# Performance work log

Measured on AMD Instinct MI355X. Metric: run time of the kernel, lower is better.

Reference implementation:

```python
import jax, jax.numpy as jnp
import numpy as np

MAX_CACHE_LEN = 4096


def _rotate_half(t):
    d = t.shape[-1] // 2
    return jnp.concatenate([-t[..., d:], t[..., :d]], axis=-1)


def _apply_rope(t, cos, sin):
    # t: (B, S, H, D); cos/sin: (S, D)
    c = cos[None, :, None, :]
    s = sin[None, :, None, :]
    return t * c + _rotate_half(t) * s


def setup_inputs() -> dict:
    key = jax.random.key(0)
    ks = jax.random.split(key, 7)
    B, S, E, D, KVH = 1, 2048, 2048, 64, 8
    sc = 0.02
    x = jax.random.normal(ks[0], (B, S, E), dtype=jnp.float32)
    Wq = jax.random.normal(ks[1], (E, E), dtype=jnp.float32) * sc
    Wk = jax.random.normal(ks[2], (KVH * D, E), dtype=jnp.float32) * sc
    Wv = jax.random.normal(ks[3], (KVH * D, E), dtype=jnp.float32) * sc
    Wo = jax.random.normal(ks[4], (E, E), dtype=jnp.float32) * sc
    # RoPE tables
    pos = jnp.arange(S, dtype=jnp.float32)[:, None]
    inv_freq = 1.0 / (10000.0 ** (jnp.arange(0, D, 2, dtype=jnp.float32) / D))
    ang = pos * inv_freq[None, :]              # (S, D/2)
    ang = jnp.concatenate([ang, ang], axis=-1)  # (S, D)
    cos = jnp.cos(ang)
    sin = jnp.sin(ang)
    # additive causal mask (1,1,S,S): 0 where allowed, -1e9 where masked
    causal = jnp.tril(jnp.ones((S, S), dtype=bool))
    attn_mask = jnp.where(causal, 0.0, -1e9).astype(jnp.float32)[None, None]
    return {"x": x, "Wq": Wq, "Wk": Wk, "Wv": Wv, "Wo": Wo,
            "cos": cos, "sin": sin, "attn_mask": attn_mask, "last_pos": S}


def reference(x, Wq, Wk, Wv, Wo, cos, sin, attn_mask, last_pos):
    B, S, E = x.shape
    D = cos.shape[-1]
    H = E // D
    KVH = Wk.shape[0] // D
    group = H // KVH

    q = (x @ Wq.T).reshape(B, S, H, D)
    k = (x @ Wk.T).reshape(B, S, KVH, D)
    v = (x @ Wv.T).reshape(B, S, KVH, D)

    q = _apply_rope(q, cos, sin)
    k = _apply_rope(k, cos, sin)

    # KV-cache write (index_copy at positions [last_pos-S, last_pos)), then slice [:last_pos]
    key_cache = jnp.zeros((B, MAX_CACHE_LEN, KVH, D), dtype=x.dtype)
    value_cache = jnp.zeros((B, MAX_CACHE_LEN, KVH, D), dtype=x.dtype)
    key_cache = jax.lax.dynamic_update_slice(key_cache, jax.lax.stop_gradient(k), (0, last_pos - S, 0, 0))
    value_cache = jax.lax.dynamic_update_slice(value_cache, jax.lax.stop_gradient(v), (0, last_pos - S, 0, 0))
    kc = key_cache[:, :last_pos]    # (B, T, KVH, D)
    vc = value_cache[:, :last_pos]

    # GQA: repeat kv heads to match q heads
    kc = jnp.repeat(kc, group, axis=2)  # (B, T, H, D)
    vc = jnp.repeat(vc, group, axis=2)

    scale = 1.0 / np.sqrt(D)
    scores = jnp.einsum('bqhd,bkhd->bhqk', q, kc) * scale
    scores = scores + attn_mask
    probs = jax.nn.softmax(scores.astype(jnp.float32), axis=-1).astype(x.dtype)
    attn = jnp.einsum('bhqk,bkhd->bqhd', probs, vc)  # (B, S, H, D)
    out = attn.reshape(B, S, E) @ Wo.T
    return out
```

## Files before the change

### kernel.cpp

```cpp
#include <hip/hip_runtime.h>
#include <stdint.h>

typedef unsigned short u16;
typedef unsigned int   u32;

typedef __bf16 bf16x8 __attribute__((ext_vector_type(8)));
typedef float  fx4    __attribute__((ext_vector_type(4)));
typedef u16    u16x8  __attribute__((ext_vector_type(8)));
typedef u16    u16x4  __attribute__((ext_vector_type(4)));

typedef __attribute__((address_space(1))) unsigned int as1_u32;
typedef __attribute__((address_space(3))) unsigned int as3_u32;

__device__ __forceinline__ void gload_lds16(const void* g, void* lds) {
  __builtin_amdgcn_global_load_lds((const as1_u32*)(uintptr_t)g,
                                   (as3_u32*)(uintptr_t)lds, 16, 0, 0);
}

__device__ __forceinline__ float b2f(u32 bits) {
  union { u32 i; float f; } v; v.i = bits << 16; return v.f;
}
__device__ __forceinline__ u16 f2b(float f) {
  union { float f; u32 i; } v; v.f = f;
  u32 x = v.i;
  return (u16)((x + 0x7fffu + ((x >> 16) & 1u)) >> 16);
}
__device__ __forceinline__ u16 f2b_hw(float f) {
  union { __bf16 b; u16 u; } v; v.b = (__bf16)f; return v.u;
}
__device__ __forceinline__ float exp2_hw(float f) {
  return __builtin_amdgcn_exp2f(f);
}
__device__ __forceinline__ u32 cvtpk_bf16(float a, float b) {
  u32 r;
  asm("v_cvt_pk_bf16_f32 %0, %1, %2" : "=v"(r) : "v"(a), "v"(b));
  return r;
}

__global__ __launch_bounds__(256) void cast_kernel(
    const float* __restrict__ s0, const float* __restrict__ s1,
    const float* __restrict__ s2, const float* __restrict__ s3,
    const float* __restrict__ s4, u16* __restrict__ dst)
{
  const size_t i8 = ((size_t)blockIdx.x * 256 + threadIdx.x) * 8;
  if (i8 >= 14680064) return;
  const float* src; size_t off;
  if      (i8 <  4194304) { src = s0; off = i8; }
  else if (i8 <  8388608) { src = s1; off = i8 - 4194304; }
  else if (i8 <  9437184) { src = s2; off = i8 - 8388608; }
  else if (i8 < 10485760) { src = s3; off = i8 - 9437184; }
  else                    { src = s4; off = i8 - 10485760; }
  const float4 a = *(const float4*)(src + off);
  const float4 b = *(const float4*)(src + off + 4);
  u16x8 o;
  o[0] = f2b(a.x); o[1] = f2b(a.y); o[2] = f2b(a.z); o[3] = f2b(a.w);
  o[4] = f2b(b.x); o[5] = f2b(b.y); o[6] = f2b(b.z); o[7] = f2b(b.w);
  *(u16x8*)(dst + i8) = o;
}

template <int MODE>
__global__ __launch_bounds__(512) void gemm_bt(
    const u16* __restrict__ A, const u16* __restrict__ B0,
    const u16* __restrict__ B1, const u16* __restrict__ B2,
    void* __restrict__ Cv, int K, int split1, int split2, int ldc,
    const float* __restrict__ cosb, const float* __restrict__ sinb,
    u16* __restrict__ vtg)
{
  __shared__ __align__(16) u16 smem[5 * 8192];

  const int n0 = blockIdx.x * 128;
  const int m0 = blockIdx.y * 128;

  const u16* Bsel; int nb;
  if (n0 < split1)      { Bsel = B0; nb = n0; }
  else if (n0 < split2) { Bsel = B1; nb = n0 - split1; }
  else                  { Bsel = B2; nb = n0 - split2; }

  const int tid  = threadIdx.x;
  const int wave = tid >> 6, lane = tid & 63;
  const int wm = wave >> 1, wn = wave & 1;
  const int quad = lane >> 4, l16 = lane & 15;

  fx4 acc[2][4];
#pragma unroll
  for (int i = 0; i < 2; ++i)
#pragma unroll
    for (int j = 0; j < 4; ++j) acc[i][j] = fx4{0.f, 0.f, 0.f, 0.f};

  const int row = tid >> 2;
  const int ch  = tid & 3;
  const int csw = (ch ^ ((row >> 1) & 3)) * 8;
  auto stage = [&](int kt, int buf) {
    u16* As = smem + buf * 8192;
    u16* Bs = As + 4096;
    const int k0 = kt * 32;
    gload_lds16(A    + (size_t)(m0 + row) * K + k0 + csw, As + tid * 8);
    gload_lds16(Bsel + (size_t)(nb + row) * K + k0 + csw, Bs + tid * 8);
  };

  const int KT = K >> 5;
  stage(0, 0); stage(1, 1); stage(2, 2); stage(3, 3);
  int bufR = 0, bufW = 4;

  const int fx = (l16 >> 1) & 3;
  const int cA = (quad ^ fx) * 8;

#pragma unroll 1
  for (int kt = 0; kt < KT; ++kt) {
    const int rem = KT - 1 - kt;
    if (rem >= 3)      asm volatile("s_waitcnt vmcnt(6)\n\ts_barrier" ::: "memory");
    else if (rem == 2) asm volatile("s_waitcnt vmcnt(4)\n\ts_barrier" ::: "memory");
    else if (rem == 1) asm volatile("s_waitcnt vmcnt(2)\n\ts_barrier" ::: "memory");
    else               asm volatile("s_waitcnt vmcnt(0)\n\ts_barrier" ::: "memory");
    if (kt + 4 < KT) stage(kt + 4, bufW);

    const u16* As = smem + bufR * 8192;
    const u16* Bs = As + 4096;

    bf16x8 af[2], bfr[4];
#pragma unroll
    for (int t = 0; t < 2; ++t)
      af[t]  = *(const bf16x8*)&As[(wm * 32 + t * 16 + l16) * 32 + cA];
#pragma unroll
    for (int t = 0; t < 4; ++t)
      bfr[t] = *(const bf16x8*)&Bs[(wn * 64 + t * 16 + l16) * 32 + cA];
#pragma unroll
    for (int ti = 0; ti < 2; ++ti)
#pragma unroll
      for (int tj = 0; tj < 4; ++tj)
        acc[ti][tj] = __builtin_amdgcn_mfma_f32_16x16x32_bf16(
            af[ti], bfr[tj], acc[ti][tj], 0, 0, 0);

    bufR = (bufR == 4) ? 0 : bufR + 1;
    bufW = (bufW == 4) ? 0 : bufW + 1;
  }

  if (MODE == 1) {
    float* C = (float*)Cv;
#pragma unroll
    for (int ti = 0; ti < 2; ++ti) {
      const int row_b = m0 + wm * 32 + ti * 16 + quad * 4;
#pragma unroll
      for (int tj = 0; tj < 4; ++tj) {
        const int col = n0 + wn * 64 + tj * 16 + l16;
#pragma unroll
        for (int r = 0; r < 4; ++r)
          C[(size_t)(row_b + r) * ldc + col] = acc[ti][tj][r];
      }
    }
  } else {
    u16* C = (u16*)Cv;
    const int cb = n0 + wn * 64;
    if (cb < 2560) {
      const float qs = (cb < 2048) ? 0.18033688f : 1.0f;
#pragma unroll
      for (int ti = 0; ti < 2; ++ti) {
#pragma unroll
        for (int r = 0; r < 4; ++r) {
          const int s = m0 + wm * 32 + ti * 16 + quad * 4 + r;
          const float* cr = cosb + s * 64;
          const float* sr = sinb + s * 64;
          u16* orow = C + (size_t)s * 3072 + cb;
#pragma unroll
          for (int tj = 0; tj < 2; ++tj) {
            const int d0 = tj * 16 + l16, d1 = d0 + 32;
            const float x0 = acc[ti][tj][r], x1 = acc[ti][tj + 2][r];
            orow[d0] = f2b((x0 * cr[d0] - x1 * sr[d0]) * qs);
            orow[d1] = f2b((x1 * cr[d1] + x0 * sr[d1]) * qs);
          }
        }
      }
    } else {
      const int vr0 = cb - 2560;
#pragma unroll
      for (int ti = 0; ti < 2; ++ti) {
        const int s0 = m0 + wm * 32 + ti * 16 + quad * 4;
#pragma unroll
        for (int tj = 0; tj < 4; ++tj) {
          const int vr = vr0 + tj * 16 + l16;
          u16x4 o;
#pragma unroll
          for (int r = 0; r < 4; ++r) o[r] = f2b(acc[ti][tj][r]);
          *(u16x4*)(vtg + (size_t)vr * 2048 + s0) = o;
        }
      }
    }
  }
}

__global__ __launch_bounds__(256) void attn_kernel(
    const u16* __restrict__ qkv, const u16* __restrict__ vt,
    u16* __restrict__ attnbuf)
{
  const int bi  = blockIdx.x;
  const int kvh = bi & 7;
  const int j   = bi >> 3;
  const int h   = kvh * 4 + (j & 3);
  const int bx  = 31 - (j >> 2);
  const int tid = threadIdx.x;
  const int w = tid >> 6, lane = tid & 63;
  const int quad = lane >> 4, l16 = lane & 15;

  __shared__ __align__(16) u16 Qs[64 * 64];
  __shared__ __align__(16) u16 Kb[2][64 * 64];
  __shared__ __align__(16) u16 Vb[2][64 * 64];
  __shared__ __align__(16) u32 Ps[4][16 * 32];

  const int r0    = bx * 64;
  const int nhalf = bx + 1;
  const int kcol  = 2048 + kvh * 64;

  const int srow = tid >> 3;
  const int sc   = tid & 7;

  auto stageQ = [&]() {
#pragma unroll
    for (int i = 0; i < 2; ++i) {
      const int r  = srow + i * 32;
      const int cs = sc ^ (r & 7);
      gload_lds16(qkv + (size_t)(r0 + r) * 3072 + h * 64 + cs * 8,
                  Qs + (size_t)(tid + i * 256) * 8);
    }
  };
  auto stageKV = [&](int n) {
    const int k0 = n * 64;
    u16* Kd = Kb[n & 1];
    u16* Vd = Vb[n & 1];
#pragma unroll
    for (int i = 0; i < 2; ++i) {
      const int r  = srow + i * 32;
      const int cs = sc ^ (r & 7);
      gload_lds16(qkv + (size_t)(k0 + r) * 3072 + kcol + cs * 8,
                  Kd + (size_t)(tid + i * 256) * 8);
      gload_lds16(vt + (size_t)(kvh * 64 + r) * 2048 + k0 + cs * 8,
                  Vd + (size_t)(tid + i * 256) * 8);
    }
  };

  stageQ();
  stageKV(0);
  asm volatile("s_waitcnt vmcnt(0)\n\ts_barrier" ::: "memory");

  const int xm = l16 & 7;
  const int qrow = w * 16 + l16;
  const bf16x8 aq0 = *(const bf16x8*)&Qs[qrow * 64 + ((quad    ) ^ xm) * 8];
  const bf16x8 aq1 = *(const bf16x8*)&Qs[qrow * 64 + ((4 + quad) ^ xm) * 8];

  fx4 O[4];
  float l_acc = 0.f;
#pragma unroll
  for (int c = 0; c < 4; ++c) O[c] = fx4{0.f, 0.f, 0.f, 0.f};

  const int s2 = (l16 & 7) << 1;

#pragma unroll 1
  for (int n = 0; n < nhalf; ++n) {
    if (n + 1 < nhalf) stageKV(n + 1);
    const u16* Kh = Kb[n & 1];
    const u16* Vd = Vb[n & 1];
    const int k0h = n * 64;

    fx4 sc4[4];
    __builtin_amdgcn_s_setprio(1);
#pragma unroll
    for (int c = 0; c < 4; ++c) {
      const int kr = c * 16 + l16;
      const bf16x8 b0 = *(const bf16x8*)&Kh[kr * 64 + ((quad    ) ^ xm) * 8];
      const bf16x8 b1 = *(const bf16x8*)&Kh[kr * 64 + ((4 + quad) ^ xm) * 8];
      fx4 z = fx4{0.f, 0.f, 0.f, 0.f};
      z      = __builtin_amdgcn_mfma_f32_16x16x32_bf16(b0, aq0, z, 0, 0, 0);
      sc4[c] = __builtin_amdgcn_mfma_f32_16x16x32_bf16(b1, aq1, z, 0, 0, 0);
    }
    __builtin_amdgcn_s_setprio(0);

    const int qg16 = r0 + w * 16 + l16;
    if (k0h >= r0) {
#pragma unroll
      for (int c = 0; c < 4; ++c)
#pragma unroll
        for (int r = 0; r < 4; ++r) {
          float p = exp2_hw(sc4[c][r]);
          if (k0h + c * 16 + quad * 4 + r > qg16) p = 0.f;
          l_acc += p;
          sc4[c][r] = p;
        }
    } else {
#pragma unroll
      for (int c = 0; c < 4; ++c)
#pragma unroll
        for (int r = 0; r < 4; ++r) {
          const float p = exp2_hw(sc4[c][r]);
          l_acc += p;
          sc4[c][r] = p;
        }
    }

#pragma unroll
    for (int c = 0; c < 4; ++c) {
      const u32 lo = cvtpk_bf16(sc4[c][0], sc4[c][1]);
      const u32 hi = cvtpk_bf16(sc4[c][2], sc4[c][3]);
      const int c2 = (c * 4 + quad) ^ s2;
      *(uint2*)&Ps[w][l16 * 32 + 2 * c2] = uint2{lo, hi};
    }

    const bf16x8 ap0 = *(const bf16x8*)&Ps[w][l16 * 32 + 2 * ((2 * quad    ) ^ s2)];
    const bf16x8 ap1 = *(const bf16x8*)&Ps[w][l16 * 32 + 2 * ((8 + 2 * quad) ^ s2)];
    __builtin_amdgcn_s_setprio(1);
#pragma unroll
    for (int c = 0; c < 4; ++c) {
      const int vr = c * 16 + l16;
      const bf16x8 v0 = *(const bf16x8*)&Vd[vr * 64 + ((quad    ) ^ xm) * 8];
      const bf16x8 v1 = *(const bf16x8*)&Vd[vr * 64 + ((4 + quad) ^ xm) * 8];
      O[c] = __builtin_amdgcn_mfma_f32_16x16x32_bf16(ap0, v0, O[c], 0, 0, 0);
      O[c] = __builtin_amdgcn_mfma_f32_16x16x32_bf16(ap1, v1, O[c], 0, 0, 0);
    }
    __builtin_amdgcn_s_setprio(0);

    asm volatile("s_waitcnt vmcnt(0)\n\ts_barrier" ::: "memory");
  }

  float l = l_acc;
  l += __shfl_xor(l, 16, 64);
  l += __shfl_xor(l, 32, 64);
  const float inv = 1.f / fmaxf(l, 1e-30f);
#pragma unroll
  for (int r = 0; r < 4; ++r) {
    const float iv = __shfl(inv, (lane & 48) | (quad * 4 + r), 64);
    const int qg = r0 + w * 16 + quad * 4 + r;
#pragma unroll
    for (int c = 0; c < 4; ++c)
      attnbuf[(size_t)qg * 2048 + h * 64 + c * 16 + l16] = f2b(O[c][r] * iv);
  }
}

extern "C" void kernel_launch(void* const* d_in, const int* in_sizes, int n_in,
                              void* d_out, int out_size, void* d_ws, size_t ws_size,
                              hipStream_t stream) {
  const float* x    = (const float*)d_in[0];
  const float* Wq   = (const float*)d_in[1];
  const float* Wk   = (const float*)d_in[2];
  const float* Wv   = (const float*)d_in[3];
  const float* Wo   = (const float*)d_in[4];
  const float* cosb = (const float*)d_in[5];
  const float* sinb = (const float*)d_in[6];
  float* out = (float*)d_out;

  u16* ws      = (u16*)d_ws;
  u16* qkv     = ws;
  u16* attnbuf = ws + 6291456;
  u16* xb      = ws + 10485760;
  u16* Wqb     = ws + 14680064;
  u16* Wkb     = ws + 18874368;
  u16* Wvb     = ws + 19922944;
  u16* Wob     = ws + 20971520;
  u16* vtg     = ws + 25165824;

  cast_kernel<<<7168, 256, 0, stream>>>(x, Wq, Wk, Wv, Wo, xb);

  gemm_bt<0><<<dim3(24, 16), 512, 0, stream>>>(
      xb, Wqb, Wkb, Wvb, qkv, 2048, 2048, 2560, 3072, cosb, sinb, vtg);

  attn_kernel<<<1024, 256, 0, stream>>>(qkv, vtg, attnbuf);

  gemm_bt<1><<<dim3(16, 16), 512, 0, stream>>>(
      attnbuf, Wob, Wob, Wob, out, 2048, 1 << 30, 1 << 30, 2048, cosb, sinb, vtg);
}
```

Baseline: 209.9 us.

## Enlarge attention query tile to 128 rows per block for K/V reuse

Each attention block now handles 128 query rows instead of 64, with every wave computing two 16-row groups, so each staged K/V tile feeds twice as many MFMAs and the grid halves to 512 blocks. Q is staged through the K buffer into registers, which frees the separate Q shared-memory array. The block-to-tile mapping is changed to pair long and short causal tiles across the two halves of the grid. This cuts global K/V traffic and barrier count per unit of work, at the cost of more registers per thread and fewer blocks to balance the causal workload.

```diff
diff --git a/kernel.cpp b/kernel.cpp
--- a/kernel.cpp
+++ b/kernel.cpp
@@ -194,34 +194,50 @@
 {
   const int bi  = blockIdx.x;
   const int kvh = bi & 7;
-  const int j   = bi >> 3;
-  const int h   = kvh * 4 + (j & 3);
-  const int bx  = 31 - (j >> 2);
+  const int hs  = (bi >> 3) & 3;
+  const int h   = kvh * 4 + hs;
+  const int g5  = bi >> 5;
+  const int qt  = (bi < 256) ? (15 - g5) : (g5 - 8);
   const int tid = threadIdx.x;
   const int w = tid >> 6, lane = tid & 63;
   const int quad = lane >> 4, l16 = lane & 15;
 
-  __shared__ __align__(16) u16 Qs[64 * 64];
   __shared__ __align__(16) u16 Kb[2][64 * 64];
   __shared__ __align__(16) u16 Vb[2][64 * 64];
-  __shared__ __align__(16) u32 Ps[4][16 * 32];
-
-  const int r0    = bx * 64;
-  const int nhalf = bx + 1;
+  __shared__ __align__(16) u32 Ps[4][2][16 * 32];
+
+  const int r0    = qt * 128;
+  const int nhalf = 2 * qt + 2;
   const int kcol  = 2048 + kvh * 64;
 
   const int srow = tid >> 3;
   const int sc   = tid & 7;
 
-  auto stageQ = [&]() {
-#pragma unroll
-    for (int i = 0; i < 2; ++i) {
+  {
+    u16* Qb = (u16*)Kb;
+#pragma unroll
+    for (int i = 0; i < 4; ++i) {
       const int r  = srow + i * 32;
       const int cs = sc ^ (r & 7);
       gload_lds16(qkv + (size_t)(r0 + r) * 3072 + h * 64 + cs * 8,
-                  Qs + (size_t)(tid + i * 256) * 8);
-    }
-  };
+                  Qb + (size_t)(tid + i * 256) * 8);
+    }
+  }
+  asm volatile("s_waitcnt vmcnt(0)\n\ts_barrier" ::: "memory");
+
+  const int xm = l16 & 7;
+  bf16x8 aq[2][2];
+  {
+    const u16* Qb = (const u16*)Kb;
+#pragma unroll
+    for (int g = 0; g < 2; ++g) {
+      const int qrow = w * 32 + g * 16 + l16;
+      aq[g][0] = *(const bf16x8*)&Qb[qrow * 64 + ((quad    ) ^ xm) * 8];
+      aq[g][1] = *(const bf16x8*)&Qb[qrow * 64 + ((4 + quad) ^ xm) * 8];
+    }
+  }
+  asm volatile("s_waitcnt lgkmcnt(0)\n\ts_barrier" ::: "memory");
+
   auto stageKV = [&](int n) {
     const int k0 = n * 64;
     u16* Kd = Kb[n & 1];
@@ -237,19 +253,15 @@
     }
   };
 
-  stageQ();
   stageKV(0);
   asm volatile("s_waitcnt vmcnt(0)\n\ts_barrier" ::: "memory");
 
-  const int xm = l16 & 7;
-  const int qrow = w * 16 + l16;
-  const bf16x8 aq0 = *(const bf16x8*)&Qs[qrow * 64 + ((quad    ) ^ xm) * 8];
-  const bf16x8 aq1 = *(const bf16x8*)&Qs[qrow * 64 + ((4 + quad) ^ xm) * 8];
-
-  fx4 O[4];
-  float l_acc = 0.f;
-#pragma unroll
-  for (int c = 0; c < 4; ++c) O[c] = fx4{0.f, 0.f, 0.f, 0.f};
+  fx4 O[2][4];
+  float l_acc[2] = {0.f, 0.f};
+#pragma unroll
+  for (int g = 0; g < 2; ++g)
+#pragma unroll
+    for (int c = 0; c < 4; ++c) O[g][c] = fx4{0.f, 0.f, 0.f, 0.f};
 
   const int s2 = (l16 & 7) << 1;
 
@@ -260,76 +272,89 @@
     const u16* Vd = Vb[n & 1];
     const int k0h = n * 64;
 
-    fx4 sc4[4];
+    fx4 sc4[2][4];
     __builtin_amdgcn_s_setprio(1);
 #pragma unroll
     for (int c = 0; c < 4; ++c) {
       const int kr = c * 16 + l16;
       const bf16x8 b0 = *(const bf16x8*)&Kh[kr * 64 + ((quad    ) ^ xm) * 8];
       const bf16x8 b1 = *(const bf16x8*)&Kh[kr * 64 + ((4 + quad) ^ xm) * 8];
-      fx4 z = fx4{0.f, 0.f, 0.f, 0.f};
-      z      = __builtin_amdgcn_mfma_f32_16x16x32_bf16(b0, aq0, z, 0, 0, 0);
-      sc4[c] = __builtin_amdgcn_mfma_f32_16x16x32_bf16(b1, aq1, z, 0, 0, 0);
+#pragma unroll
+      for (int g = 0; g < 2; ++g) {
+        fx4 z = fx4{0.f, 0.f, 0.f, 0.f};
+        z         = __builtin_amdgcn_mfma_f32_16x16x32_bf16(b0, aq[g][0], z, 0, 0, 0);
+        sc4[g][c] = __builtin_amdgcn_mfma_f32_16x16x32_bf16(b1, aq[g][1], z, 0, 0, 0);
+      }
     }
     __builtin_amdgcn_s_setprio(0);
 
-    const int qg16 = r0 + w * 16 + l16;
-    if (k0h >= r0) {
-#pragma unroll
-      for (int c = 0; c < 4; ++c)
-#pragma unroll
-        for (int r = 0; r < 4; ++r) {
-          float p = exp2_hw(sc4[c][r]);
-          if (k0h + c * 16 + quad * 4 + r > qg16) p = 0.f;
-          l_acc += p;
-          sc4[c][r] = p;
-        }
-    } else {
-#pragma unroll
-      for (int c = 0; c < 4; ++c)
-#pragma unroll
-        for (int r = 0; r < 4; ++r) {
-          const float p = exp2_hw(sc4[c][r]);
-          l_acc += p;
-          sc4[c][r] = p;
-        }
-    }
-
-#pragma unroll
-    for (int c = 0; c < 4; ++c) {
-      const u32 lo = cvtpk_bf16(sc4[c][0], sc4[c][1]);
-      const u32 hi = cvtpk_bf16(sc4[c][2], sc4[c][3]);
-      const int c2 = (c * 4 + quad) ^ s2;
-      *(uint2*)&Ps[w][l16 * 32 + 2 * c2] = uint2{lo, hi};
-    }
-
-    const bf16x8 ap0 = *(const bf16x8*)&Ps[w][l16 * 32 + 2 * ((2 * quad    ) ^ s2)];
-    const bf16x8 ap1 = *(const bf16x8*)&Ps[w][l16 * 32 + 2 * ((8 + 2 * quad) ^ s2)];
+#pragma unroll
+    for (int g = 0; g < 2; ++g) {
+      const int qbase = r0 + w * 32 + g * 16;
+      const int qg16  = qbase + l16;
+      if (k0h + 63 > qbase) {
+#pragma unroll
+        for (int c = 0; c < 4; ++c)
+#pragma unroll
+          for (int r = 0; r < 4; ++r) {
+            float p = exp2_hw(sc4[g][c][r]);
+            if (k0h + c * 16 + quad * 4 + r > qg16) p = 0.f;
+            l_acc[g] += p;
+            sc4[g][c][r] = p;
+          }
+      } else {
+#pragma unroll
+        for (int c = 0; c < 4; ++c)
+#pragma unroll
+          for (int r = 0; r < 4; ++r) {
+            const float p = exp2_hw(sc4[g][c][r]);
+            l_acc[g] += p;
+            sc4[g][c][r] = p;
+          }
+      }
+#pragma unroll
+      for (int c = 0; c < 4; ++c) {
+        const u32 lo = cvtpk_bf16(sc4[g][c][0], sc4[g][c][1]);
+        const u32 hi = cvtpk_bf16(sc4[g][c][2], sc4[g][c][3]);
+        const int c2 = (c * 4 + quad) ^ s2;
+        *(uint2*)&Ps[w][g][l16 * 32 + 2 * c2] = uint2{lo, hi};
+      }
+    }
+
+    const bf16x8 ap00 = *(const bf16x8*)&Ps[w][0][l16 * 32 + 2 * ((2 * quad    ) ^ s2)];
+    const bf16x8 ap01 = *(const bf16x8*)&Ps[w][0][l16 * 32 + 2 * ((8 + 2 * quad) ^ s2)];
+    const bf16x8 ap10 = *(const bf16x8*)&Ps[w][1][l16 * 32 + 2 * ((2 * quad    ) ^ s2)];
+    const bf16x8 ap11 = *(const bf16x8*)&Ps[w][1][l16 * 32 + 2 * ((8 + 2 * quad) ^ s2)];
     __builtin_amdgcn_s_setprio(1);
 #pragma unroll
     for (int c = 0; c < 4; ++c) {
       const int vr = c * 16 + l16;
       const bf16x8 v0 = *(const bf16x8*)&Vd[vr * 64 + ((quad    ) ^ xm) * 8];
       const bf16x8 v1 = *(const bf16x8*)&Vd[vr * 64 + ((4 + quad) ^ xm) * 8];
-      O[c] = __builtin_amdgcn_mfma_f32_16x16x32_bf16(ap0, v0, O[c], 0, 0, 0);
-      O[c] = __builtin_amdgcn_mfma_f32_16x16x32_bf16(ap1, v1, O[c], 0, 0, 0);
+      O[0][c] = __builtin_amdgcn_mfma_f32_16x16x32_bf16(ap00, v0, O[0][c], 0, 0, 0);
+      O[0][c] = __builtin_amdgcn_mfma_f32_16x16x32_bf16(ap01, v1, O[0][c], 0, 0, 0);
+      O[1][c] = __builtin_amdgcn_mfma_f32_16x16x32_bf16(ap10, v0, O[1][c], 0, 0, 0);
+      O[1][c] = __builtin_amdgcn_mfma_f32_16x16x32_bf16(ap11, v1, O[1][c], 0, 0, 0);
     }
     __builtin_amdgcn_s_setprio(0);
 
     asm volatile("s_waitcnt vmcnt(0)\n\ts_barrier" ::: "memory");
   }
 
-  float l = l_acc;
-  l += __shfl_xor(l, 16, 64);
-  l += __shfl_xor(l, 32, 64);
-  const float inv = 1.f / fmaxf(l, 1e-30f);
-#pragma unroll
-  for (int r = 0; r < 4; ++r) {
-    const float iv = __shfl(inv, (lane & 48) | (quad * 4 + r), 64);
-    const int qg = r0 + w * 16 + quad * 4 + r;
-#pragma unroll
-    for (int c = 0; c < 4; ++c)
-      attnbuf[(size_t)qg * 2048 + h * 64 + c * 16 + l16] = f2b(O[c][r] * iv);
+#pragma unroll
+  for (int g = 0; g < 2; ++g) {
+    float l = l_acc[g];
+    l += __shfl_xor(l, 16, 64);
+    l += __shfl_xor(l, 32, 64);
+    const float inv = 1.f / fmaxf(l, 1e-30f);
+#pragma unroll
+    for (int r = 0; r < 4; ++r) {
+      const float iv = __shfl(inv, (lane & 48) | (quad * 4 + r), 64);
+      const int qg = r0 + w * 32 + g * 16 + quad * 4 + r;
+#pragma unroll
+      for (int c = 0; c < 4; ++c)
+        attnbuf[(size_t)qg * 2048 + h * 64 + c * 16 + l16] = f2b(O[g][c][r] * iv);
+    }
   }
 }
 
@@ -360,7 +385,7 @@
   gemm_bt<0><<<dim3(24, 16), 512, 0, stream>>>(
       xb, Wqb, Wkb, Wvb, qkv, 2048, 2048, 2560, 3072, cosb, sinb, vtg);
 
-  attn_kernel<<<1024, 256, 0, stream>>>(qkv, vtg, attnbuf);
+  attn_kernel<<<512, 256, 0, stream>>>(qkv, vtg, attnbuf);
 
   gemm_bt<1><<<dim3(16, 16), 512, 0, stream>>>(
       attnbuf, Wob, Wob, Wob, out, 2048, 1 << 30, 1 << 30, 2048, cosb, sinb, vtg);
```

Result: slower. 218.2 us (+4.0%).
